# Kernel optimization log

Measured on AMD Instinct MI355X. Metric: run time of the kernel, lower is better.

The kernel has to match this reference:

```python
import jax, jax.numpy as jnp
import numpy as np

MIMO_RANK = 4  # module constant; q/k are identical across rank and mimo_v=mimo_out=ones,
               # q_bias=k_bias=0, so the rank sum equals MIMO_RANK * single-rank output.


def _rotary(t, ang):
    # split-half rotary: t [..., d], ang [..., d//2]
    d2 = t.shape[-1] // 2
    t1, t2 = t[..., :d2], t[..., d2:]
    c, s = jnp.cos(ang), jnp.sin(ang)
    return jnp.concatenate([t1 * c - t2 * s, t1 * s + t2 * c], axis=-1)


def setup_inputs() -> dict:
    key = jax.random.key(0)
    ks = jax.random.split(key, 6)
    b, l, h, dv, g, dqk = 2, 4096, 32, 64, 1, 128
    x = jax.random.normal(ks[0], (b, l, h, dv), jnp.float32)
    # positive step sizes (discretization dt)
    dt = jax.random.uniform(ks[1], (b, l, h), jnp.float32) * 0.05 + 1e-3
    # negative decay rates so exp(A*dt) < 1
    A = -(jax.random.uniform(ks[2], (h,), jnp.float32) + 0.5)
    B_gate = jax.random.normal(ks[3], (b, l, g, dqk), jnp.float32)
    C_gate = jax.random.normal(ks[4], (b, l, g, dqk), jnp.float32)
    D = jax.random.normal(ks[5], (h,), jnp.float32)
    return {"x": x, "dt": dt, "A": A, "B_gate": B_gate, "C_gate": C_gate,
            "D": D, "chunk_size": 64}


def reference(x, dt, A, B_gate, C_gate, D, chunk_size):
    # Mamba3 MIMO chunked selective scan (SSD) with rotary QK decay.
    # Recurrence per (b, h):  H_t = exp(A_h*dt_t) * H_{t-1} + rot(k_t) (dt_t x_t)^T
    #                         y_t = rot(q_t)^T H_t * MIMO_RANK + D_h * x_t
    # where q=C_gate, k=B_gate (shared across heads, ngroups=1) and the rotary
    # angle is theta_t = cumsum(dt) (TILELANG_ROTARY_DIV=2 -> dqk//2 angles).
    b, l, h, dv = x.shape
    dqk = C_gate.shape[-1]
    c = chunk_size
    n = l // c

    ang = jnp.cumsum(dt, axis=1)[..., None]                     # [b,l,h,1]
    ang = jnp.broadcast_to(ang, (b, l, h, dqk // 2))
    q = jnp.broadcast_to(C_gate[:, :, 0, :][:, :, None, :], (b, l, h, dqk))
    k = jnp.broadcast_to(B_gate[:, :, 0, :][:, :, None, :], (b, l, h, dqk))
    rotq = _rotary(q, ang)                                      # [b,l,h,dqk]
    rotk = _rotary(k, ang)
    adt = A[None, None, :] * dt                                 # [b,l,h] log-decay

    chunk = lambda t: t.reshape(b, n, c, *t.shape[2:])
    rq, rk = chunk(rotq), chunk(rotk)                           # [b,n,c,h,dqk]
    u = chunk(dt[..., None] * x)                                # [b,n,c,h,dv]
    a = chunk(adt)                                              # [b,n,c,h]
    cum = jnp.cumsum(a, axis=2)                                 # within-chunk cum log-decay

    # ---- intra-chunk (quadratic within chunk) ----
    seg = cum[:, :, :, None, :] - cum[:, :, None, :, :]         # [b,n,t,s,h]
    mask = jnp.tril(jnp.ones((c, c), bool))
    L = jnp.where(mask[None, None, :, :, None], jnp.exp(seg), 0.0)
    S = jnp.einsum('bnthd,bnshd->bntsh', rq, rk)                # [b,n,t,s,h]
    y_intra = jnp.einsum('bntsh,bnshe->bnthe', S * L, u)        # [b,n,c,h,dv]

    # ---- inter-chunk state recurrence ----
    decay_to_end = jnp.exp(cum[:, :, -1:, :] - cum)             # [b,n,c,h]
    dH = jnp.einsum('bnshd,bnsh,bnshe->bnhde', rk, decay_to_end, u)  # [b,n,h,dqk,dv]
    cdecay = jnp.exp(cum[:, :, -1, :])                          # [b,n,h] full-chunk decay

    def step(H, inp):
        dc, dh = inp
        Hprev = H
        return dc[:, :, None, None] * H + dh, Hprev

    H0 = jnp.zeros((b, h, dqk, dv), x.dtype)
    _, Hprev = jax.lax.scan(step, H0,
                            (jnp.moveaxis(cdecay, 1, 0), jnp.moveaxis(dH, 1, 0)))
    Hprev = jnp.moveaxis(Hprev, 0, 1)                           # [b,n,h,dqk,dv]

    y_inter = jnp.einsum('bnthd,bnth,bnhde->bnthe', rq, jnp.exp(cum), Hprev)

    y = MIMO_RANK * (y_intra + y_inter).reshape(b, l, h, dv)
    return y + D[None, None, :, None] * x
```

## Files before the change

### kernel.cpp

```cpp
#include <hip/hip_runtime.h>
#include <hip/hip_bf16.h>

#define BB 2
#define LL 4096
#define HH 32
#define DV 64
#define DQK 128
#define CC 64
#define NN 64
#define MIMO_RANK 4.0f

typedef __attribute__((ext_vector_type(8))) short short8;
typedef __attribute__((ext_vector_type(4))) float f32x4;

__device__ __forceinline__ ushort f2bf(float f) {
    uint u = __float_as_uint(f);
    u += 0x7FFF + ((u >> 16) & 1);
    return (ushort)(u >> 16);
}
__device__ __forceinline__ float bfbits2f(uint lo16) {
    return __uint_as_float(lo16 << 16);
}
__device__ __forceinline__ uint pkbf2(float lo, float hi) {
    return (uint)f2bf(lo) | ((uint)f2bf(hi) << 16);
}
union U8 { uint u[4]; short8 s; };

__device__ __forceinline__ int rk_off(int s, int d) {
    return s * 128 + (((((d >> 3) & 15) ^ (s & 7)) << 3)) + (d & 7);
}
__device__ __forceinline__ int rkT_off(int d, int s) {
    return d * 64 + ((((s >> 3) ^ (d & 7)) & 7) << 3) + (s & 7);
}
__device__ __forceinline__ int uwT_off(int e, int s) {
    return e * 64 + ((((s >> 3) ^ (e & 7)) & 7) << 3) + (s & 7);
}
__device__ __forceinline__ int fSL(int t) {
    return (((t & 3) << 1) ^ ((t >> 2) & 7)) & 7;
}
__device__ __forceinline__ int SL_off(int t, int s) {
    return t * 64 + ((((s >> 3) ^ fSL(t)) & 7) << 3) + (s & 7);
}

__device__ __forceinline__ void make_rot_frags(const float* __restrict__ G,
                                               size_t gb, float cv, float sv,
                                               int kgrp, short8* fr) {
    #pragma unroll
    for (int kk = 0; kk < 4; ++kk) {
        int d0 = kk * 32 + kgrp;
        int dl = d0 & 63;
        bool low = d0 < 64;
        float4 a1 = *(const float4*)(G + gb + dl);
        float4 b1 = *(const float4*)(G + gb + dl + 4);
        float4 a2 = *(const float4*)(G + gb + dl + 64);
        float4 b2 = *(const float4*)(G + gb + dl + 68);
        float v0, v1, v2, v3, v4, v5, v6, v7;
        if (low) {
            v0 = a1.x * cv - a2.x * sv; v1 = a1.y * cv - a2.y * sv;
            v2 = a1.z * cv - a2.z * sv; v3 = a1.w * cv - a2.w * sv;
            v4 = b1.x * cv - b2.x * sv; v5 = b1.y * cv - b2.y * sv;
            v6 = b1.z * cv - b2.z * sv; v7 = b1.w * cv - b2.w * sv;
        } else {
            v0 = a1.x * sv + a2.x * cv; v1 = a1.y * sv + a2.y * cv;
            v2 = a1.z * sv + a2.z * cv; v3 = a1.w * sv + a2.w * cv;
            v4 = b1.x * sv + b2.x * cv; v5 = b1.y * sv + b2.y * cv;
            v6 = b1.z * sv + b2.z * cv; v7 = b1.w * sv + b2.w * cv;
        }
        U8 r;
        r.u[0] = pkbf2(v0, v1); r.u[1] = pkbf2(v2, v3);
        r.u[2] = pkbf2(v4, v5); r.u[3] = pkbf2(v6, v7);
        fr[kk] = r.s;
    }
}

__global__ __launch_bounds__(256) void k_scan_dt(const float* __restrict__ dt,
                                                 float* __restrict__ ang) {
    int bh = blockIdx.x;
    int b = bh / HH, h = bh % HH;
    int tid = threadIdx.x;
    const int PT = LL / 256;
    float v[PT];
    float s = 0.f;
    int tbase = tid * PT;
    for (int i = 0; i < PT; ++i) {
        v[i] = dt[(((size_t)b * LL + tbase + i) * HH) + h];
        s += v[i];
    }
    int lane = tid & 63, wv = tid >> 6;
    float ps = s;
    for (int off = 1; off < 64; off <<= 1) {
        float o = __shfl_up(ps, off, 64);
        if (lane >= off) ps += o;
    }
    __shared__ float wsum[4];
    if (lane == 63) wsum[wv] = ps;
    __syncthreads();
    float wadd = 0.f;
    for (int w = 0; w < wv; ++w) wadd += wsum[w];
    float run = wadd + ps - s;
    for (int i = 0; i < PT; ++i) {
        run += v[i];
        ang[(((size_t)b * LL + tbase + i) * HH) + h] = run;
    }
}

__global__ __launch_bounds__(256, 4) void k_intra(
    const float* __restrict__ x, const float* __restrict__ dt,
    const float* __restrict__ A, const float* __restrict__ Bg,
    const float* __restrict__ Cg, const float* __restrict__ ang,
    const float* __restrict__ Dd,
    float* __restrict__ out, ushort* __restrict__ dH,
    float* __restrict__ cdecay) {
    int n = blockIdx.x, h = blockIdx.y, b = blockIdx.z;
    int tid = threadIdx.x;
    int t0 = n * CC;

    __shared__ ushort rkS[CC * DQK];
    __shared__ ushort rkT[DQK * CC];
    __shared__ ushort uwT[DV * CC];

    int wv = tid >> 6, lane = tid & 63;
    int lrow = lane & 15;
    int g = lane >> 4;
    int kgrp = g * 8;
    int orow = g * 4;

    float Ah = A[h];
    size_t angBase = ((size_t)b * LL + t0) * HH + h;
    float aend = ang[angBase + 63 * HH];

    if (tid == 0) {
        float angPrev = (t0 == 0) ? 0.f : ang[angBase - HH];
        cdecay[(b * NN + n) * HH + h] = __expf(Ah * (aend - angPrev));
    }

    const float* BgRow = Bg + ((size_t)b * LL + t0) * DQK;

    #pragma unroll
    for (int it = 0; it < 2; ++it) {
        int w = tid + 256 * it;
        int s = w >> 3, oct = w & 7;
        float a = ang[angBase + (size_t)s * HH];
        float sv, cv;
        __sincosf(a, &sv, &cv);
        const float* p = BgRow + s * DQK + 8 * oct;
        float4 a0 = *(const float4*)(p);
        float4 a1 = *(const float4*)(p + 4);
        float4 b0 = *(const float4*)(p + 64);
        float4 b1 = *(const float4*)(p + 68);
        U8 lo, hi;
        lo.u[0] = pkbf2(a0.x * cv - b0.x * sv, a0.y * cv - b0.y * sv);
        lo.u[1] = pkbf2(a0.z * cv - b0.z * sv, a0.w * cv - b0.w * sv);
        lo.u[2] = pkbf2(a1.x * cv - b1.x * sv, a1.y * cv - b1.y * sv);
        lo.u[3] = pkbf2(a1.z * cv - b1.z * sv, a1.w * cv - b1.w * sv);
        hi.u[0] = pkbf2(a0.x * sv + b0.x * cv, a0.y * sv + b0.y * cv);
        hi.u[1] = pkbf2(a0.z * sv + b0.z * cv, a0.w * sv + b0.w * cv);
        hi.u[2] = pkbf2(a1.x * sv + b1.x * cv, a1.y * sv + b1.y * cv);
        hi.u[3] = pkbf2(a1.z * sv + b1.z * cv, a1.w * sv + b1.w * cv);
        *(short8*)&rkS[rk_off(s, 8 * oct)] = lo.s;
        *(short8*)&rkS[rk_off(s, 8 * oct + 64)] = hi.s;
    }

    #pragma unroll
    for (int it = 0; it < 2; ++it) {
        int w = tid + 256 * it;
        int e = w & 63;
        int s0 = 8 * (w >> 6);
        U8 pk;
        #pragma unroll
        for (int jp = 0; jp < 4; ++jp) {
            int s_a = s0 + 2 * jp, s_b = s_a + 1;
            float dwA = dt[(((size_t)b * LL + t0 + s_a) * HH) + h] *
                        __expf(Ah * (aend - ang[angBase + (size_t)s_a * HH]));
            float dwB = dt[(((size_t)b * LL + t0 + s_b) * HH) + h] *
                        __expf(Ah * (aend - ang[angBase + (size_t)s_b * HH]));
            float xa = x[((((size_t)b * LL + t0 + s_a) * HH) + h) * DV + e] * dwA;
            float xb = x[((((size_t)b * LL + t0 + s_b) * HH) + h) * DV + e] * dwB;
            pk.u[jp] = pkbf2(xa, xb);
        }
        *(short8*)&uwT[uwT_off(e, s0)] = pk.s;
    }

    int t_own = 16 * wv + lrow;
    float a_town = ang[angBase + (size_t)t_own * HH];
    float cvq, svq;
    __sincosf(a_town, &svq, &cvq);
    short8 aq[4];
    make_rot_frags(Cg, ((size_t)b * LL + t0 + t_own) * DQK, cvq, svq, kgrp, aq);

    __syncthreads();

    #pragma unroll
    for (int it = 0; it < 4; ++it) {
        int w = tid + 256 * it;
        int d = w & 127, soct = w >> 7;
        int s0 = 8 * soct;
        uint v[8];
        #pragma unroll
        for (int j = 0; j < 8; ++j) v[j] = rkS[rk_off(s0 + j, d)];
        U8 pk;
        pk.u[0] = v[0] | (v[1] << 16);
        pk.u[1] = v[2] | (v[3] << 16);
        pk.u[2] = v[4] | (v[5] << 16);
        pk.u[3] = v[6] | (v[7] << 16);
        *(short8*)&rkT[rkT_off(d, s0)] = pk.s;
    }

    f32x4 accS[4] = {{0.f,0.f,0.f,0.f},{0.f,0.f,0.f,0.f},
                     {0.f,0.f,0.f,0.f},{0.f,0.f,0.f,0.f}};
    #pragma unroll
    for (int kk = 0; kk < 4; ++kk) {
        #pragma unroll
        for (int nt = 0; nt < 4; ++nt) {
            int s = 16 * nt + lrow;
            const short8 bfr = *(const short8*)&rkS[rk_off(s, 32 * kk + kgrp)];
            accS[nt] = __builtin_amdgcn_mfma_f32_16x16x32_bf16(
                aq[kk], bfr, accS[nt], 0, 0, 0);
        }
    }

    __syncthreads();

    ushort* SLs = rkS;
    #pragma unroll
    for (int rr = 0; rr < 4; ++rr) {
        int t = 16 * wv + orow + rr;
        float etv = __expf(Ah * (ang[angBase + (size_t)t * HH] - aend));
        #pragma unroll
        for (int nt = 0; nt < 4; ++nt) {
            int s = 16 * nt + lrow;
            float v = (t >= s) ? accS[nt][rr] * etv : 0.f;
            SLs[SL_off(t, s)] = f2bf(v);
        }
    }

    __syncthreads();

    {
        f32x4 accY[4] = {{0.f,0.f,0.f,0.f},{0.f,0.f,0.f,0.f},
                         {0.f,0.f,0.f,0.f},{0.f,0.f,0.f,0.f}};
        #pragma unroll
        for (int kk = 0; kk < 2; ++kk) {
            const short8 a = *(const short8*)&SLs[SL_off(16 * wv + lrow, 32 * kk + kgrp)];
            #pragma unroll
            for (int nt = 0; nt < 4; ++nt) {
                const short8 bfr = *(const short8*)&uwT[uwT_off(16 * nt + lrow, 32 * kk + kgrp)];
                accY[nt] = __builtin_amdgcn_mfma_f32_16x16x32_bf16(
                    a, bfr, accY[nt], 0, 0, 0);
            }
        }
        float Dh = Dd[h];
        #pragma unroll
        for (int nt = 0; nt < 4; ++nt) {
            int e = 16 * nt + lrow;
            #pragma unroll
            for (int rr = 0; rr < 4; ++rr) {
                int t = 16 * wv + orow + rr;
                size_t oidx = ((((size_t)b * LL + t0 + t) * HH) + h) * DV + e;
                out[oidx] = MIMO_RANK * accY[nt][rr] + Dh * x[oidx];
            }
        }
    }

    {
        f32x4 accH[2][4] = {{{0.f,0.f,0.f,0.f},{0.f,0.f,0.f,0.f},
                             {0.f,0.f,0.f,0.f},{0.f,0.f,0.f,0.f}},
                            {{0.f,0.f,0.f,0.f},{0.f,0.f,0.f,0.f},
                             {0.f,0.f,0.f,0.f},{0.f,0.f,0.f,0.f}}};
        #pragma unroll
        for (int kk = 0; kk < 2; ++kk) {
            #pragma unroll
            for (int mt = 0; mt < 2; ++mt) {
                const short8 a = *(const short8*)&rkT[rkT_off(32 * wv + 16 * mt + lrow, 32 * kk + kgrp)];
                #pragma unroll
                for (int nt = 0; nt < 4; ++nt) {
                    const short8 bfr = *(const short8*)&uwT[uwT_off(16 * nt + lrow, 32 * kk + kgrp)];
                    accH[mt][nt] = __builtin_amdgcn_mfma_f32_16x16x32_bf16(
                        a, bfr, accH[mt][nt], 0, 0, 0);
                }
            }
        }
        ushort* dHp = dH + (((size_t)(b * NN + n) * HH) + h) * (DQK * DV);
        #pragma unroll
        for (int q = 0; q < 4; ++q) {
            int mt = q >> 1, np = q & 1;
            U8 st;
            st.u[0] = pkbf2(accH[mt][2 * np][0], accH[mt][2 * np][1]);
            st.u[1] = pkbf2(accH[mt][2 * np][2], accH[mt][2 * np][3]);
            st.u[2] = pkbf2(accH[mt][2 * np + 1][0], accH[mt][2 * np + 1][1]);
            st.u[3] = pkbf2(accH[mt][2 * np + 1][2], accH[mt][2 * np + 1][3]);
            *(short8*)(dHp + ((size_t)(wv * 4 + q) * 64 + lane) * 8) = st.s;
        }
    }
}

__global__ __launch_bounds__(256) void k_scan_chunks(
    uint* __restrict__ dH, const float* __restrict__ cdecay) {
    uint f = blockIdx.x * 256 + threadIdx.x;
    int b = (int)(f >> 17);
    uint r = f & 0x1FFFF;
    int h = (int)((r >> 12) & 31);
    uint base = ((uint)b << 23) | r;
    const float* cd = cdecay + (size_t)b * NN * HH + h;
    float h0 = 0.f, h1 = 0.f;
    for (int n = 0; n < NN; ++n) {
        uint a = base + ((uint)n << 17);
        uint v = dH[a];
        float v0 = bfbits2f(v & 0xFFFF), v1 = bfbits2f(v >> 16);
        dH[a] = pkbf2(h0, h1);
        float c = cd[n * HH];
        h0 = c * h0 + v0;
        h1 = c * h1 + v1;
    }
}

__global__ __launch_bounds__(256, 4) void k_inter(
    const float* __restrict__ A, const float* __restrict__ Cg,
    const float* __restrict__ ang, const ushort* __restrict__ Hprev,
    float* __restrict__ out) {
    int n = blockIdx.x, h = blockIdx.y, b = blockIdx.z;
    int tid = threadIdx.x;
    int t0 = n * CC;

    __shared__ __align__(16) uint Hp[16 * 260];
    __shared__ float csv[CC], ssv[CC], gs[CC], angs[CC];
    __shared__ float angPrev_s;

    float Ah = A[h];
    if (tid < CC) {
        float a = ang[(((size_t)b * LL + t0 + tid) * HH) + h];
        angs[tid] = a;
        float sv, cv;
        __sincosf(a, &sv, &cv);
        csv[tid] = cv;
        ssv[tid] = sv;
    }
    if (tid == 0)
        angPrev_s = (t0 == 0) ? 0.f : ang[(((size_t)b * LL + t0 - 1) * HH) + h];
    __syncthreads();
    if (tid < CC) gs[tid] = __expf(Ah * (angs[tid] - angPrev_s));

    const uint* Hsrc = (const uint*)(Hprev + (((size_t)(b * NN + n) * HH) + h) * (DQK * DV));
    #pragma unroll
    for (int it = 0; it < 4; ++it) {
        int p = tid + 256 * it;
        uint4 v = *(const uint4*)(Hsrc + (size_t)p * 4);
        int row = p >> 6, c = p & 63;
        uint4* Hrow = (uint4*)&Hp[row * 260];
        Hrow[c] = v;
    }

    int wv = tid >> 6, lane = tid & 63;
    int lrow = lane & 15;
    int g2 = lane >> 4;
    int kgrp = g2 * 8;
    int orow = g2 * 4;

    int t_own = 16 * wv + lrow;
    short8 aq[4];
    make_rot_frags(Cg, ((size_t)b * LL + t0 + t_own) * DQK,
                   csv[t_own], ssv[t_own], kgrp, aq);
    __syncthreads();

    f32x4 accI[4] = {{0.f,0.f,0.f,0.f},{0.f,0.f,0.f,0.f},
                     {0.f,0.f,0.f,0.f},{0.f,0.f,0.f,0.f}};
    int mt = g2 >> 1;
    int gp0 = 2 * (g2 & 1);
    #pragma unroll
    for (int kk = 0; kk < 4; ++kk) {
        #pragma unroll
        for (int nt = 0; nt < 4; ++nt) {
            int q = mt * 2 + (nt >> 1);
            int row = kk * 4 + q;
            int sb = (nt & 1) * 2;
            const uint2 u0 = *(const uint2*)&Hp[row * 260 + (16 * gp0 + lrow) * 4 + sb];
            const uint2 u1 = *(const uint2*)&Hp[row * 260 + (16 * (gp0 + 1) + lrow) * 4 + sb];
            U8 fr;
            fr.u[0] = u0.x; fr.u[1] = u0.y; fr.u[2] = u1.x; fr.u[3] = u1.y;
            accI[nt] = __builtin_amdgcn_mfma_f32_16x16x32_bf16(
                aq[kk], fr.s, accI[nt], 0, 0, 0);
        }
    }

    #pragma unroll
    for (int rr = 0; rr < 4; ++rr) {
        int t = 16 * wv + orow + rr;
        float g4 = MIMO_RANK * gs[t];
        #pragma unroll
        for (int nt = 0; nt < 4; ++nt) {
            int e = 16 * nt + lrow;
            size_t oidx = ((((size_t)b * LL + t0 + t) * HH) + h) * DV + e;
            out[oidx] += g4 * accI[nt][rr];
        }
    }
}

extern "C" void kernel_launch(void* const* d_in, const int* in_sizes, int n_in,
                              void* d_out, int out_size, void* d_ws,
                              size_t ws_size, hipStream_t stream) {
    (void)in_sizes; (void)n_in; (void)out_size; (void)ws_size;
    const float* x  = (const float*)d_in[0];
    const float* dt = (const float*)d_in[1];
    const float* A  = (const float*)d_in[2];
    const float* Bg = (const float*)d_in[3];
    const float* Cg = (const float*)d_in[4];
    const float* Dd = (const float*)d_in[5];
    float* out = (float*)d_out;
    float* ws  = (float*)d_ws;

    float*  ang    = ws;
    float*  cdecay = ws + 262144;
    ushort* dH     = (ushort*)(ws + 266240);

    k_scan_dt<<<BB * HH, 256, 0, stream>>>(dt, ang);
    k_intra<<<dim3(NN, HH, BB), 256, 0, stream>>>(x, dt, A, Bg, Cg, ang, Dd,
                                                  out, dH, cdecay);
    k_scan_chunks<<<(BB * HH * DQK * DV / 2) / 256, 256, 0, stream>>>(
        (uint*)dH, cdecay);
    k_inter<<<dim3(NN, HH, BB), 256, 0, stream>>>(A, Cg, ang, dH, out);
}
```

Baseline: 116.6 us.

## Precompute per-timestep rotary/decay table in scan kernel and drop LDS transpose

Result: slower. 126.7 us (+8.7%).

```diff
diff --git a/kernel.cpp b/kernel.cpp
--- a/kernel.cpp
+++ b/kernel.cpp
@@ -28,9 +28,6 @@
 
 __device__ __forceinline__ int rk_off(int s, int d) {
     return s * 128 + (((((d >> 3) & 15) ^ (s & 7)) << 3)) + (d & 7);
-}
-__device__ __forceinline__ int rkT_off(int d, int s) {
-    return d * 64 + ((((s >> 3) ^ (d & 7)) & 7) << 3) + (s & 7);
 }
 __device__ __forceinline__ int uwT_off(int e, int s) {
     return e * 64 + ((((s >> 3) ^ (e & 7)) & 7) << 3) + (s & 7);
@@ -74,7 +71,9 @@
 }
 
 __global__ __launch_bounds__(256) void k_scan_dt(const float* __restrict__ dt,
-                                                 float* __restrict__ ang) {
+                                                 const float* __restrict__ A,
+                                                 float4* __restrict__ tbl,
+                                                 float* __restrict__ cdecay) {
     int bh = blockIdx.x;
     int b = bh / HH, h = bh % HH;
     int tid = threadIdx.x;
@@ -97,26 +96,37 @@
     __syncthreads();
     float wadd = 0.f;
     for (int w = 0; w < wv; ++w) wadd += wsum[w];
-    float run = wadd + ps - s;
+    float run0 = wadd + ps - s;
+    float run_end = run0 + s;
+    float aend  = __shfl(run_end, lane | 3, 64);
+    float aprev = __shfl(run0, lane & ~3, 64);
+    float Ah = A[h];
+    if ((tid & 3) == 0) {
+        int n = tid >> 2;
+        cdecay[(b * NN + n) * HH + h] = __expf(Ah * (aend - aprev));
+    }
+    float4* tb = tbl + ((size_t)(b * HH + h) * LL) + tbase;
+    float run = run0;
     for (int i = 0; i < PT; ++i) {
         run += v[i];
-        ang[(((size_t)b * LL + tbase + i) * HH) + h] = run;
-    }
-}
-
-__global__ __launch_bounds__(256, 4) void k_intra(
-    const float* __restrict__ x, const float* __restrict__ dt,
-    const float* __restrict__ A, const float* __restrict__ Bg,
-    const float* __restrict__ Cg, const float* __restrict__ ang,
+        float sv, cv;
+        __sincosf(run, &sv, &cv);
+        float dw = __expf(Ah * (aend - run));
+        float et = __expf(Ah * (run - aend));
+        tb[i] = make_float4(cv, sv, v[i] * dw, et);
+    }
+}
+
+__global__ __launch_bounds__(256, 6) void k_intra(
+    const float* __restrict__ x, const float* __restrict__ Bg,
+    const float* __restrict__ Cg, const float4* __restrict__ tbl,
     const float* __restrict__ Dd,
-    float* __restrict__ out, ushort* __restrict__ dH,
-    float* __restrict__ cdecay) {
+    float* __restrict__ out, ushort* __restrict__ dH) {
     int n = blockIdx.x, h = blockIdx.y, b = blockIdx.z;
     int tid = threadIdx.x;
     int t0 = n * CC;
 
     __shared__ ushort rkS[CC * DQK];
-    __shared__ ushort rkT[DQK * CC];
     __shared__ ushort uwT[DV * CC];
 
     int wv = tid >> 6, lane = tid & 63;
@@ -125,24 +135,15 @@
     int kgrp = g * 8;
     int orow = g * 4;
 
-    float Ah = A[h];
-    size_t angBase = ((size_t)b * LL + t0) * HH + h;
-    float aend = ang[angBase + 63 * HH];
-
-    if (tid == 0) {
-        float angPrev = (t0 == 0) ? 0.f : ang[angBase - HH];
-        cdecay[(b * NN + n) * HH + h] = __expf(Ah * (aend - angPrev));
-    }
-
+    const float4* tb = tbl + ((size_t)(b * HH + h) * LL) + t0;
     const float* BgRow = Bg + ((size_t)b * LL + t0) * DQK;
 
     #pragma unroll
     for (int it = 0; it < 2; ++it) {
         int w = tid + 256 * it;
         int s = w >> 3, oct = w & 7;
-        float a = ang[angBase + (size_t)s * HH];
-        float sv, cv;
-        __sincosf(a, &sv, &cv);
+        float4 tv = tb[s];
+        float cv = tv.x, sv = tv.y;
         const float* p = BgRow + s * DQK + 8 * oct;
         float4 a0 = *(const float4*)(p);
         float4 a1 = *(const float4*)(p + 4);
@@ -170,10 +171,8 @@
         #pragma unroll
         for (int jp = 0; jp < 4; ++jp) {
             int s_a = s0 + 2 * jp, s_b = s_a + 1;
-            float dwA = dt[(((size_t)b * LL + t0 + s_a) * HH) + h] *
-                        __expf(Ah * (aend - ang[angBase + (size_t)s_a * HH]));
-            float dwB = dt[(((size_t)b * LL + t0 + s_b) * HH) + h] *
-                        __expf(Ah * (aend - ang[angBase + (size_t)s_b * HH]));
+            float dwA = tb[s_a].z;
+            float dwB = tb[s_b].z;
             float xa = x[((((size_t)b * LL + t0 + s_a) * HH) + h) * DV + e] * dwA;
             float xb = x[((((size_t)b * LL + t0 + s_b) * HH) + h) * DV + e] * dwB;
             pk.u[jp] = pkbf2(xa, xb);
@@ -182,29 +181,11 @@
     }
 
     int t_own = 16 * wv + lrow;
-    float a_town = ang[angBase + (size_t)t_own * HH];
-    float cvq, svq;
-    __sincosf(a_town, &svq, &cvq);
+    float4 tq = tb[t_own];
     short8 aq[4];
-    make_rot_frags(Cg, ((size_t)b * LL + t0 + t_own) * DQK, cvq, svq, kgrp, aq);
+    make_rot_frags(Cg, ((size_t)b * LL + t0 + t_own) * DQK, tq.x, tq.y, kgrp, aq);
 
     __syncthreads();
-
-    #pragma unroll
-    for (int it = 0; it < 4; ++it) {
-        int w = tid + 256 * it;
-        int d = w & 127, soct = w >> 7;
-        int s0 = 8 * soct;
-        uint v[8];
-        #pragma unroll
-        for (int j = 0; j < 8; ++j) v[j] = rkS[rk_off(s0 + j, d)];
-        U8 pk;
-        pk.u[0] = v[0] | (v[1] << 16);
-        pk.u[1] = v[2] | (v[3] << 16);
-        pk.u[2] = v[4] | (v[5] << 16);
-        pk.u[3] = v[6] | (v[7] << 16);
-        *(short8*)&rkT[rkT_off(d, s0)] = pk.s;
-    }
 
     f32x4 accS[4] = {{0.f,0.f,0.f,0.f},{0.f,0.f,0.f,0.f},
                      {0.f,0.f,0.f,0.f},{0.f,0.f,0.f,0.f}};
@@ -219,13 +200,32 @@
         }
     }
 
+    short8 aH[2][2];
+    #pragma unroll
+    for (int kk = 0; kk < 2; ++kk) {
+        #pragma unroll
+        for (int mt = 0; mt < 2; ++mt) {
+            int d = 32 * wv + 16 * mt + lrow;
+            uint vv[8];
+            #pragma unroll
+            for (int j = 0; j < 8; ++j)
+                vv[j] = rkS[rk_off(32 * kk + kgrp + j, d)];
+            U8 pk;
+            pk.u[0] = vv[0] | (vv[1] << 16);
+            pk.u[1] = vv[2] | (vv[3] << 16);
+            pk.u[2] = vv[4] | (vv[5] << 16);
+            pk.u[3] = vv[6] | (vv[7] << 16);
+            aH[kk][mt] = pk.s;
+        }
+    }
+
     __syncthreads();
 
     ushort* SLs = rkS;
     #pragma unroll
     for (int rr = 0; rr < 4; ++rr) {
         int t = 16 * wv + orow + rr;
-        float etv = __expf(Ah * (ang[angBase + (size_t)t * HH] - aend));
+        float etv = tb[t].w;
         #pragma unroll
         for (int nt = 0; nt < 4; ++nt) {
             int s = 16 * nt + lrow;
@@ -271,12 +271,11 @@
         for (int kk = 0; kk < 2; ++kk) {
             #pragma unroll
             for (int mt = 0; mt < 2; ++mt) {
-                const short8 a = *(const short8*)&rkT[rkT_off(32 * wv + 16 * mt + lrow, 32 * kk + kgrp)];
                 #pragma unroll
                 for (int nt = 0; nt < 4; ++nt) {
                     const short8 bfr = *(const short8*)&uwT[uwT_off(16 * nt + lrow, 32 * kk + kgrp)];
                     accH[mt][nt] = __builtin_amdgcn_mfma_f32_16x16x32_bf16(
-                        a, bfr, accH[mt][nt], 0, 0, 0);
+                        aH[kk][mt], bfr, accH[mt][nt], 0, 0, 0);
                 }
             }
         }
@@ -314,31 +313,18 @@
     }
 }
 
-__global__ __launch_bounds__(256, 4) void k_inter(
-    const float* __restrict__ A, const float* __restrict__ Cg,
-    const float* __restrict__ ang, const ushort* __restrict__ Hprev,
+__global__ __launch_bounds__(256, 6) void k_inter(
+    const float* __restrict__ Cg, const float4* __restrict__ tbl,
+    const float* __restrict__ cdecay, const ushort* __restrict__ Hprev,
     float* __restrict__ out) {
     int n = blockIdx.x, h = blockIdx.y, b = blockIdx.z;
     int tid = threadIdx.x;
     int t0 = n * CC;
 
     __shared__ __align__(16) uint Hp[16 * 260];
-    __shared__ float csv[CC], ssv[CC], gs[CC], angs[CC];
-    __shared__ float angPrev_s;
-
-    float Ah = A[h];
-    if (tid < CC) {
-        float a = ang[(((size_t)b * LL + t0 + tid) * HH) + h];
-        angs[tid] = a;
-        float sv, cv;
-        __sincosf(a, &sv, &cv);
-        csv[tid] = cv;
-        ssv[tid] = sv;
-    }
-    if (tid == 0)
-        angPrev_s = (t0 == 0) ? 0.f : ang[(((size_t)b * LL + t0 - 1) * HH) + h];
-    __syncthreads();
-    if (tid < CC) gs[tid] = __expf(Ah * (angs[tid] - angPrev_s));
+
+    const float4* tb = tbl + ((size_t)(b * HH + h) * LL) + t0;
+    float cdec = cdecay[(b * NN + n) * HH + h];
 
     const uint* Hsrc = (const uint*)(Hprev + (((size_t)(b * NN + n) * HH) + h) * (DQK * DV));
     #pragma unroll
@@ -357,9 +343,9 @@
     int orow = g2 * 4;
 
     int t_own = 16 * wv + lrow;
+    float4 tq = tb[t_own];
     short8 aq[4];
-    make_rot_frags(Cg, ((size_t)b * LL + t0 + t_own) * DQK,
-                   csv[t_own], ssv[t_own], kgrp, aq);
+    make_rot_frags(Cg, ((size_t)b * LL + t0 + t_own) * DQK, tq.x, tq.y, kgrp, aq);
     __syncthreads();
 
     f32x4 accI[4] = {{0.f,0.f,0.f,0.f},{0.f,0.f,0.f,0.f},
@@ -385,7 +371,7 @@
     #pragma unroll
     for (int rr = 0; rr < 4; ++rr) {
         int t = 16 * wv + orow + rr;
-        float g4 = MIMO_RANK * gs[t];
+        float g4 = MIMO_RANK * tb[t].w * cdec;
         #pragma unroll
         for (int nt = 0; nt < 4; ++nt) {
             int e = 16 * nt + lrow;
@@ -408,14 +394,13 @@
     float* out = (float*)d_out;
     float* ws  = (float*)d_ws;
 
-    float*  ang    = ws;
-    float*  cdecay = ws + 262144;
-    ushort* dH     = (ushort*)(ws + 266240);
-
-    k_scan_dt<<<BB * HH, 256, 0, stream>>>(dt, ang);
-    k_intra<<<dim3(NN, HH, BB), 256, 0, stream>>>(x, dt, A, Bg, Cg, ang, Dd,
-                                                  out, dH, cdecay);
+    float4* tbl    = (float4*)ws;
+    float*  cdecay = ws + (size_t)BB * HH * LL * 4;
+    ushort* dH     = (ushort*)(cdecay + BB * NN * HH);
+
+    k_scan_dt<<<BB * HH, 256, 0, stream>>>(dt, A, tbl, cdecay);
+    k_intra<<<dim3(NN, HH, BB), 256, 0, stream>>>(x, Bg, Cg, tbl, Dd, out, dH);
     k_scan_chunks<<<(BB * HH * DQK * DV / 2) / 256, 256, 0, stream>>>(
         (uint*)dH, cdecay);
-    k_inter<<<dim3(NN, HH, BB), 256, 0, stream>>>(A, Cg, ang, dH, out);
-}
+    k_inter<<<dim3(NN, HH, BB), 256, 0, stream>>>(Cg, tbl, cdecay, dH, out);
+}
```
